# Performance work log

Hardware: AMD Instinct MI355X
Metric: run time of the kernel (lower is better)

## Reference

```python
import jax, jax.numpy as jnp
import numpy as np

B, F, D = 16384, 256, 128
H = [512, 256]
OUT = 8
VOCAB = 100000


def setup_inputs() -> dict:
    key = jax.random.key(0)
    ks = jax.random.split(key, 16)
    s = lambda k, *sh: jax.random.normal(k, sh, jnp.float32) * 0.05
    return dict(
        features=jax.random.normal(ks[0], (B, F), jnp.float32),
        ent_idx=jax.random.randint(ks[1], (B,), 0, VOCAB),
        target=jax.random.randint(ks[2], (B,), 0, OUT),
        Wf=s(ks[3], F, D), bf=jnp.zeros((D,), jnp.float32),
        Wu=s(ks[4], D, D), bu=jnp.zeros((D,), jnp.float32),
        w_cf=s(ks[5], D), w_fc=s(ks[6], D),
        w_ef=s(ks[7], D), w_fe=s(ks[8], D),
        b_c=jnp.zeros((1,), jnp.float32), b_e=jnp.zeros((1,), jnp.float32),
        head_tab=s(ks[9], VOCAB, D), ent_tab=s(ks[10], VOCAB, D),
        W0=s(ks[11], 2 * D, H[0]), b0=jnp.zeros((H[0],), jnp.float32),
        W1=s(ks[12], H[0], H[1]), b1=jnp.zeros((H[1],), jnp.float32),
        W2=s(ks[13], H[1], OUT), b2=jnp.zeros((OUT,), jnp.float32),
    )


def cross_compress(f, e, w_cf, w_fc, w_ef, w_fe, b_c, b_e):
    # torch code builds c = f (outer) e of shape (B,D,D) then matmuls a (D,1)
    # vector; algebraically (f e^T) w = f * (e . w), so we use the O(B*D) form.
    ew_cf = e @ w_cf  # (B,)
    fw_fc = f @ w_fc
    ew_ef = e @ w_ef
    fw_fe = f @ w_fe
    new_f = f * ew_cf[:, None] + e * fw_fc[:, None] + b_c
    new_e = f * ew_ef[:, None] + e * fw_fe[:, None] + b_e
    return new_f, new_e


def reference(features, ent_idx, target, Wf, bf, Wu, bu, w_cf, w_fc, w_ef,
              w_fe, b_c, b_e, head_tab, ent_tab, W0, b0, W1, b1, W2, b2):
    # 'rec' branch of CompanyOperationEvaluation.forward (eval mode, dropout=id)
    cf = jax.nn.relu(features @ Wf + bf)          # feature_layer
    e = ent_tab[ent_idx]                           # entity_embed lookup
    h = head_tab[ent_idx]                          # head_embed lookup (same ids)
    for _ in range(2):
        cf = jax.nn.relu(cf @ Wu + bu)             # user_low_mlp_layer
        h, e = cross_compress(h, e, w_cf, w_fc, w_ef, w_fe, b_c, b_e)
    high = jnp.concatenate([cf, e], axis=1)        # (B, 2D)
    x = jax.nn.relu(high @ W0 + b0)
    x = jax.nn.relu(x @ W1 + b1)
    x = jax.nn.relu(x @ W2 + b2)                   # pred_last_layer
    prob = jax.nn.softmax(x, axis=1)
    return (prob, target)
```

## Files before the change

### kernel.cpp

```cpp
#include <hip/hip_runtime.h>
#include <hip/hip_bf16.h>


typedef __bf16 bf16x8 __attribute__((ext_vector_type(8)));
typedef float floatx4 __attribute__((ext_vector_type(4)));

__device__ __forceinline__ unsigned short f2bf(float x) {
  unsigned int u = __builtin_bit_cast(unsigned int, x);
  u = (u + 0x7FFFu + ((u >> 16) & 1u)) >> 16;
  return (unsigned short)u;
}

__global__ __launch_bounds__(256) void prep_kernel(
    const int* __restrict__ ent_idx, const float* __restrict__ head_tab,
    const float* __restrict__ ent_tab,
    const float* __restrict__ w_cf, const float* __restrict__ w_fc,
    const float* __restrict__ w_ef, const float* __restrict__ w_fe,
    const float* __restrict__ b_c, const float* __restrict__ b_e,
    const float* __restrict__ Wf, const float* __restrict__ Wu,
    const float* __restrict__ W0, const float* __restrict__ W1,
    const float* __restrict__ W2,
    unsigned short* __restrict__ high,
    unsigned short* __restrict__ wfT, unsigned short* __restrict__ wuT,
    unsigned short* __restrict__ w0T, unsigned short* __restrict__ w1T,
    unsigned short* __restrict__ w2T) {
  __shared__ unsigned short tile[32][34];
  const int bid = blockIdx.x, tid = threadIdx.x;
  if (bid < 2048) {
    const int row = bid * 8 + (tid >> 5);
    const int c = (tid & 31) * 4;
    const int idx = ent_idx[row];
    float4 hv = *(const float4*)(head_tab + (size_t)idx * 128 + c);
    float4 ev = *(const float4*)(ent_tab + (size_t)idx * 128 + c);
    float h[4] = {hv.x, hv.y, hv.z, hv.w};
    float e[4] = {ev.x, ev.y, ev.z, ev.w};
    float wcf[4], wfc[4], wef[4], wfe[4];
#pragma unroll
    for (int j = 0; j < 4; ++j) {
      wcf[j] = w_cf[c + j]; wfc[j] = w_fc[c + j];
      wef[j] = w_ef[c + j]; wfe[j] = w_fe[c + j];
    }
    const float bc = b_c[0], be = b_e[0];
#pragma unroll
    for (int it = 0; it < 2; ++it) {
      float d0 = 0, d1 = 0, d2 = 0, d3 = 0;
#pragma unroll
      for (int j = 0; j < 4; ++j) {
        d0 += e[j] * wcf[j]; d1 += h[j] * wfc[j];
        d2 += e[j] * wef[j]; d3 += h[j] * wfe[j];
      }
#pragma unroll
      for (int s = 1; s < 32; s <<= 1) {
        d0 += __shfl_xor(d0, s); d1 += __shfl_xor(d1, s);
        d2 += __shfl_xor(d2, s); d3 += __shfl_xor(d3, s);
      }
      float nh[4], ne[4];
#pragma unroll
      for (int j = 0; j < 4; ++j) {
        nh[j] = h[j] * d0 + e[j] * d1 + bc;
        ne[j] = h[j] * d2 + e[j] * d3 + be;
      }
#pragma unroll
      for (int j = 0; j < 4; ++j) { h[j] = nh[j]; e[j] = ne[j]; }
    }
    uint2 v;
    v.x = (unsigned)f2bf(e[0]) | ((unsigned)f2bf(e[1]) << 16);
    v.y = (unsigned)f2bf(e[2]) | ((unsigned)f2bf(e[3]) << 16);
    *(uint2*)(high + (size_t)row * 256 + 128 + c) = v;
  } else if (bid < 2352) {
    int t = bid - 2048;
    const float* src; unsigned short* dst; int N, K, kt, nt;
    if (t < 32)       { src = Wf; dst = wfT; N = 128; K = 256; kt = t >> 2;       nt = t & 3; }
    else if (t < 48)  { t -= 32;  src = Wu; dst = wuT; N = 128; K = 128; kt = t >> 2; nt = t & 3; }
    else if (t < 176) { t -= 48;  src = W0; dst = w0T; N = 512; K = 256; kt = t >> 4; nt = t & 15; }
    else              { t -= 176; src = W1; dst = w1T; N = 256; K = 512; kt = t >> 3; nt = t & 7; }
    {
      int r = tid >> 3, cg = (tid & 7) * 4;
      float4 v = *(const float4*)(src + (size_t)(kt * 32 + r) * N + nt * 32 + cg);
      tile[r][cg + 0] = f2bf(v.x); tile[r][cg + 1] = f2bf(v.y);
      tile[r][cg + 2] = f2bf(v.z); tile[r][cg + 3] = f2bf(v.w);
    }
    __syncthreads();
    {
      int rp = tid >> 3, cg = (tid & 7) * 4;
      uint2 o;
      o.x = (unsigned)tile[cg + 0][rp] | ((unsigned)tile[cg + 1][rp] << 16);
      o.y = (unsigned)tile[cg + 2][rp] | ((unsigned)tile[cg + 3][rp] << 16);
      *(uint2*)(dst + (size_t)(nt * 32 + rp) * K + kt * 32 + cg) = o;
    }
  } else {
#pragma unroll
    for (int i = 0; i < 8; ++i) {
      int g = tid * 8 + i, k = g >> 3, n = g & 7;
      w2T[n * 256 + k] = f2bf(W2[g]);
    }
  }
}

template <int LDA>
__device__ __forceinline__ void layer32(const unsigned short* A_sh,
                                        const unsigned short* __restrict__ BT,
                                        int K, unsigned short* b_sh,
                                        floatx4 acc[2][2]) {
  const int tid = threadIdx.x, lane = tid & 63, wave = tid >> 6;
  const int m16 = lane & 15, quad = lane >> 4;
#pragma unroll
  for (int mi = 0; mi < 2; ++mi)
#pragma unroll
    for (int ni = 0; ni < 2; ++ni) acc[mi][ni] = (floatx4){0.f, 0.f, 0.f, 0.f};
  for (int k0 = 0; k0 < K; k0 += 64) {
    __syncthreads();
#pragma unroll
    for (int i = 0; i < 4; ++i) {
      int chunk = i * 256 + tid;
      int row = chunk >> 3, seg = chunk & 7;
      *(uint4*)&b_sh[row * 72 + seg * 8] =
          *(const uint4*)(BT + (size_t)row * K + k0 + seg * 8);
    }
    __syncthreads();
#pragma unroll
    for (int kk = 0; kk < 64; kk += 32) {
      bf16x8 a[2], b[2];
#pragma unroll
      for (int mi = 0; mi < 2; ++mi)
        a[mi] = *(const bf16x8*)&A_sh[(mi * 16 + m16) * LDA + k0 + kk + quad * 8];
#pragma unroll
      for (int ni = 0; ni < 2; ++ni)
        b[ni] = *(const bf16x8*)&b_sh[(wave * 32 + ni * 16 + m16) * 72 + kk + quad * 8];
#pragma unroll
      for (int mi = 0; mi < 2; ++mi)
#pragma unroll
        for (int ni = 0; ni < 2; ++ni)
          acc[mi][ni] = __builtin_amdgcn_mfma_f32_16x16x32_bf16(a[mi], b[ni], acc[mi][ni], 0, 0, 0);
    }
  }
  __syncthreads();
}

__global__ __launch_bounds__(256) void cf_chain_kernel(
    const float* __restrict__ features, const unsigned short* __restrict__ wfT,
    const unsigned short* __restrict__ wuT, const float* __restrict__ bf_,
    const float* __restrict__ bu, unsigned short* __restrict__ high) {
  __shared__ __align__(16) unsigned short feat_sh[32 * 264];
  __shared__ __align__(16) unsigned short buf0[32 * 136];
  __shared__ __align__(16) unsigned short buf1[32 * 136];
  __shared__ __align__(16) unsigned short b_sh[128 * 72];
  const int tid = threadIdx.x;
  const int r0 = blockIdx.x * 32;
#pragma unroll
  for (int i = 0; i < 8; ++i) {
    int idx4 = i * 256 + tid;
    int row = idx4 >> 6, c = (idx4 & 63) * 4;
    float4 v = *(const float4*)(features + (size_t)(r0 + row) * 256 + c);
    uint2 o;
    o.x = (unsigned)f2bf(v.x) | ((unsigned)f2bf(v.y) << 16);
    o.y = (unsigned)f2bf(v.z) | ((unsigned)f2bf(v.w) << 16);
    *(uint2*)&feat_sh[row * 264 + c] = o;
  }
  const int lane = tid & 63, wave = tid >> 6;
  const int m16 = lane & 15, quad = lane >> 4;
  floatx4 acc[2][2];

  layer32<264>(feat_sh, wfT, 256, b_sh, acc);
#pragma unroll
  for (int mi = 0; mi < 2; ++mi)
#pragma unroll
    for (int ni = 0; ni < 2; ++ni) {
      int col = wave * 32 + ni * 16 + m16;
      float bv = bf_[col];
#pragma unroll
      for (int r = 0; r < 4; ++r)
        buf0[(mi * 16 + quad * 4 + r) * 136 + col] =
            f2bf(fmaxf(acc[mi][ni][r] + bv, 0.f));
    }
  layer32<136>(buf0, wuT, 128, b_sh, acc);
#pragma unroll
  for (int mi = 0; mi < 2; ++mi)
#pragma unroll
    for (int ni = 0; ni < 2; ++ni) {
      int col = wave * 32 + ni * 16 + m16;
      float bv = bu[col];
#pragma unroll
      for (int r = 0; r < 4; ++r)
        buf1[(mi * 16 + quad * 4 + r) * 136 + col] =
            f2bf(fmaxf(acc[mi][ni][r] + bv, 0.f));
    }
  layer32<136>(buf1, wuT, 128, b_sh, acc);
#pragma unroll
  for (int mi = 0; mi < 2; ++mi)
#pragma unroll
    for (int ni = 0; ni < 2; ++ni) {
      int col = wave * 32 + ni * 16 + m16;
      float bv = bu[col];
#pragma unroll
      for (int r = 0; r < 4; ++r) {
        int row = r0 + mi * 16 + quad * 4 + r;
        high[(size_t)row * 256 + col] = f2bf(fmaxf(acc[mi][ni][r] + bv, 0.f));
      }
    }
}

__global__ __launch_bounds__(256) void gemm128_kernel(
    const unsigned short* __restrict__ A, const unsigned short* __restrict__ BT,
    const float* __restrict__ bias, unsigned short* __restrict__ C,
    int K, int ldc) {
  __shared__ __align__(16) unsigned short a_sh[128 * 72];
  __shared__ __align__(16) unsigned short b_sh[128 * 72];
  const int tid = threadIdx.x;
  const int bn = blockIdx.x, bm = blockIdx.y;
  const int lane = tid & 63;
  const int wave = tid >> 6;
  const int wm = wave & 1, wn = wave >> 1;
  const int m16 = lane & 15, quad = lane >> 4;

  floatx4 acc[4][4];
#pragma unroll
  for (int i = 0; i < 4; ++i)
#pragma unroll
    for (int j = 0; j < 4; ++j) acc[i][j] = (floatx4){0.f, 0.f, 0.f, 0.f};

  for (int k0 = 0; k0 < K; k0 += 64) {
    __syncthreads();
#pragma unroll
    for (int i = 0; i < 4; ++i) {
      int chunk = i * 256 + tid;
      int row = chunk >> 3, seg = chunk & 7;
      *(uint4*)&a_sh[row * 72 + seg * 8] =
          *(const uint4*)(A + (size_t)(bm * 128 + row) * K + k0 + seg * 8);
      *(uint4*)&b_sh[row * 72 + seg * 8] =
          *(const uint4*)(BT + (size_t)(bn * 128 + row) * K + k0 + seg * 8);
    }
    __syncthreads();
#pragma unroll
    for (int kk = 0; kk < 64; kk += 32) {
      bf16x8 af[4], bfr[4];
#pragma unroll
      for (int mi = 0; mi < 4; ++mi)
        af[mi] = *(const bf16x8*)&a_sh[(wm * 64 + mi * 16 + m16) * 72 + kk + quad * 8];
#pragma unroll
      for (int ni = 0; ni < 4; ++ni)
        bfr[ni] = *(const bf16x8*)&b_sh[(wn * 64 + ni * 16 + m16) * 72 + kk + quad * 8];
#pragma unroll
      for (int mi = 0; mi < 4; ++mi)
#pragma unroll
        for (int ni = 0; ni < 4; ++ni)
          acc[mi][ni] = __builtin_amdgcn_mfma_f32_16x16x32_bf16(
              af[mi], bfr[ni], acc[mi][ni], 0, 0, 0);
    }
  }
#pragma unroll
  for (int mi = 0; mi < 4; ++mi) {
#pragma unroll
    for (int ni = 0; ni < 4; ++ni) {
      int col = bn * 128 + wn * 64 + ni * 16 + m16;
      float bv = bias[col];
#pragma unroll
      for (int r = 0; r < 4; ++r) {
        int row = bm * 128 + wm * 64 + mi * 16 + quad * 4 + r;
        C[(size_t)row * ldc + col] = f2bf(fmaxf(acc[mi][ni][r] + bv, 0.f));
      }
    }
  }
}

__global__ __launch_bounds__(256) void gemm_w1_final_kernel(
    const unsigned short* __restrict__ x0, const unsigned short* __restrict__ w1T,
    const float* __restrict__ b1, const unsigned short* __restrict__ w2T,
    const float* __restrict__ b2, const int* __restrict__ target,
    float* __restrict__ out) {
  __shared__ __align__(16) unsigned short a_sh[32 * 72];
  __shared__ __align__(16) unsigned short b_sh[256 * 72];
  __shared__ __align__(16) unsigned short w2_sh[2048];
  unsigned short* x1_sh = b_sh;
  const int tid = threadIdx.x;
  const int r0 = blockIdx.x * 32;
  *(uint4*)&w2_sh[tid * 8] = *(const uint4*)(w2T + tid * 8);
  const int lane = tid & 63, wave = tid >> 6;
  const int m16 = lane & 15, quad = lane >> 4;
  floatx4 acc[2][4];
#pragma unroll
  for (int mi = 0; mi < 2; ++mi)
#pragma unroll
    for (int ni = 0; ni < 4; ++ni) acc[mi][ni] = (floatx4){0.f, 0.f, 0.f, 0.f};

  for (int k0 = 0; k0 < 512; k0 += 64) {
    __syncthreads();
    {
      int row = tid >> 3, seg = tid & 7;
      *(uint4*)&a_sh[row * 72 + seg * 8] =
          *(const uint4*)(x0 + (size_t)(r0 + row) * 512 + k0 + seg * 8);
    }
#pragma unroll
    for (int i = 0; i < 8; ++i) {
      int chunk = i * 256 + tid;
      int row = chunk >> 3, seg = chunk & 7;
      *(uint4*)&b_sh[row * 72 + seg * 8] =
          *(const uint4*)(w1T + (size_t)row * 512 + k0 + seg * 8);
    }
    __syncthreads();
#pragma unroll
    for (int kk = 0; kk < 64; kk += 32) {
      bf16x8 a[2], b[4];
#pragma unroll
      for (int mi = 0; mi < 2; ++mi)
        a[mi] = *(const bf16x8*)&a_sh[(mi * 16 + m16) * 72 + kk + quad * 8];
#pragma unroll
      for (int ni = 0; ni < 4; ++ni)
        b[ni] = *(const bf16x8*)&b_sh[(wave * 64 + ni * 16 + m16) * 72 + kk + quad * 8];
#pragma unroll
      for (int mi = 0; mi < 2; ++mi)
#pragma unroll
        for (int ni = 0; ni < 4; ++ni)
          acc[mi][ni] = __builtin_amdgcn_mfma_f32_16x16x32_bf16(a[mi], b[ni], acc[mi][ni], 0, 0, 0);
    }
  }
  __syncthreads();
#pragma unroll
  for (int mi = 0; mi < 2; ++mi)
#pragma unroll
    for (int ni = 0; ni < 4; ++ni) {
      int col = wave * 64 + ni * 16 + m16;
      float bv = b1[col];
#pragma unroll
      for (int r = 0; r < 4; ++r)
        x1_sh[(mi * 16 + quad * 4 + r) * 264 + col] = f2bf(fmaxf(acc[mi][ni][r] + bv, 0.f));
    }
  __syncthreads();
  {
    int row = tid >> 3, q = tid & 7;
    float p[8];
#pragma unroll
    for (int n = 0; n < 8; ++n) p[n] = 0.f;
#pragma unroll
    for (int jb = 0; jb < 4; ++jb) {
      bf16x8 xv = *(const bf16x8*)&x1_sh[row * 264 + q * 32 + jb * 8];
#pragma unroll
      for (int n = 0; n < 8; ++n) {
        bf16x8 wv = *(const bf16x8*)&w2_sh[n * 256 + q * 32 + jb * 8];
#pragma unroll
        for (int j = 0; j < 8; ++j) p[n] += (float)xv[j] * (float)wv[j];
      }
    }
#pragma unroll
    for (int s = 1; s < 8; s <<= 1)
#pragma unroll
      for (int n = 0; n < 8; ++n) p[n] += __shfl_xor(p[n], s);
    if (q == 0) {
      float mx = -1e30f;
#pragma unroll
      for (int n = 0; n < 8; ++n) {
        p[n] = fmaxf(p[n] + b2[n], 0.f);
        mx = fmaxf(mx, p[n]);
      }
      float sum = 0.f;
#pragma unroll
      for (int n = 0; n < 8; ++n) { p[n] = __expf(p[n] - mx); sum += p[n]; }
      const float inv = 1.f / sum;
      const int gr = r0 + row;
      float4 o0 = {p[0] * inv, p[1] * inv, p[2] * inv, p[3] * inv};
      float4 o1 = {p[4] * inv, p[5] * inv, p[6] * inv, p[7] * inv};
      *(float4*)(out + (size_t)gr * 8) = o0;
      *(float4*)(out + (size_t)gr * 8 + 4) = o1;
      out[16384 * 8 + gr] = (float)target[gr];
    }
  }
}

extern "C" void kernel_launch(void* const* d_in, const int* in_sizes, int n_in,
                              void* d_out, int out_size, void* d_ws, size_t ws_size,
                              hipStream_t stream) {
  const float* features = (const float*)d_in[0];
  const int* ent_idx    = (const int*)d_in[1];
  const int* target     = (const int*)d_in[2];
  const float* Wf  = (const float*)d_in[3];
  const float* bf_ = (const float*)d_in[4];
  const float* Wu  = (const float*)d_in[5];
  const float* bu  = (const float*)d_in[6];
  const float* w_cf = (const float*)d_in[7];
  const float* w_fc = (const float*)d_in[8];
  const float* w_ef = (const float*)d_in[9];
  const float* w_fe = (const float*)d_in[10];
  const float* b_c  = (const float*)d_in[11];
  const float* b_e  = (const float*)d_in[12];
  const float* head_tab = (const float*)d_in[13];
  const float* ent_tab  = (const float*)d_in[14];
  const float* W0 = (const float*)d_in[15];
  const float* b0 = (const float*)d_in[16];
  const float* W1 = (const float*)d_in[17];
  const float* b1 = (const float*)d_in[18];
  const float* W2 = (const float*)d_in[19];
  const float* b2 = (const float*)d_in[20];
  float* out = (float*)d_out;

  unsigned short* ws = (unsigned short*)d_ws;
  size_t off = 0;
  auto alloc = [&](size_t n) { unsigned short* p = ws + off; off += n; return p; };
  unsigned short* high = alloc(16384ull * 256);
  unsigned short* x0   = alloc(16384ull * 512);
  unsigned short* wfT  = alloc(32768);
  unsigned short* wuT  = alloc(16384);
  unsigned short* w0T  = alloc(131072);
  unsigned short* w1T  = alloc(131072);
  unsigned short* w2T  = alloc(2048);
  (void)ws_size; (void)in_sizes; (void)n_in; (void)out_size;

  prep_kernel<<<2353, 256, 0, stream>>>(ent_idx, head_tab, ent_tab,
      w_cf, w_fc, w_ef, w_fe, b_c, b_e, Wf, Wu, W0, W1, W2,
      high, wfT, wuT, w0T, w1T, w2T);
  cf_chain_kernel<<<512, 256, 0, stream>>>(features, wfT, wuT, bf_, bu, high);
  gemm128_kernel<<<dim3(4, 128), 256, 0, stream>>>(high, w0T, b0, x0, 256, 512);
  gemm_w1_final_kernel<<<512, 256, 0, stream>>>(x0, w1T, b1, w2T, b2, target, out);
}
```

Measured before the change: 191.0 us.

## Fuse cf chain, W0 GEMM and W1/final layers into one per-row-block kernel

Merges the cf_chain, W0 GEMM, and W1+softmax kernels into a single kernel working on 32-row blocks. The cf output and the x0 activations stay in shared memory instead of going through global memory, which removes the 16384x512 x0 round trip and two launches. The cost is that each block now reloads the full W0 and W1 weights from global/L2 with a small M tile (32 rows). Shared memory per block also grows, which may lower occupancy.

```diff
diff --git a/kernel.cpp b/kernel.cpp
--- a/kernel.cpp
+++ b/kernel.cpp
@@ -137,16 +137,28 @@
   __syncthreads();
 }
 
-__global__ __launch_bounds__(256) void cf_chain_kernel(
+__global__ __launch_bounds__(256) void fused_mlp_kernel(
     const float* __restrict__ features, const unsigned short* __restrict__ wfT,
     const unsigned short* __restrict__ wuT, const float* __restrict__ bf_,
-    const float* __restrict__ bu, unsigned short* __restrict__ high) {
-  __shared__ __align__(16) unsigned short feat_sh[32 * 264];
-  __shared__ __align__(16) unsigned short buf0[32 * 136];
-  __shared__ __align__(16) unsigned short buf1[32 * 136];
-  __shared__ __align__(16) unsigned short b_sh[128 * 72];
+    const float* __restrict__ bu, const unsigned short* __restrict__ high,
+    const unsigned short* __restrict__ w0T, const float* __restrict__ b0,
+    const unsigned short* __restrict__ w1T, const float* __restrict__ b1,
+    const unsigned short* __restrict__ w2T, const float* __restrict__ b2,
+    const int* __restrict__ target, float* __restrict__ out) {
+  __shared__ __align__(16) unsigned short regionA[17152];
+  __shared__ __align__(16) unsigned short b_sh[256 * 72];
+  __shared__ __align__(16) unsigned short w2_sh[2048];
+  unsigned short* feat_sh = regionA;
+  unsigned short* buf0 = regionA + 8448;
+  unsigned short* buf1 = regionA + 12800;
+  unsigned short* A_sh = regionA;
+  unsigned short* x0_sh = regionA;
+  unsigned short* x1_sh = b_sh;
+
   const int tid = threadIdx.x;
   const int r0 = blockIdx.x * 32;
+  *(uint4*)&w2_sh[tid * 8] = *(const uint4*)(w2T + tid * 8);
+
 #pragma unroll
   for (int i = 0; i < 8; ++i) {
     int idx4 = i * 256 + tid;
@@ -173,6 +185,13 @@
         buf0[(mi * 16 + quad * 4 + r) * 136 + col] =
             f2bf(fmaxf(acc[mi][ni][r] + bv, 0.f));
     }
+#pragma unroll
+  for (int i = 0; i < 2; ++i) {
+    int idx = i * 256 + tid;
+    int row = idx >> 4, seg = idx & 15;
+    *(uint4*)&A_sh[row * 264 + 128 + seg * 8] =
+        *(const uint4*)(high + (size_t)(r0 + row) * 256 + 128 + seg * 8);
+  }
   layer32<136>(buf0, wuT, 128, b_sh, acc);
 #pragma unroll
   for (int mi = 0; mi < 2; ++mi)
@@ -193,103 +212,68 @@
       int col = wave * 32 + ni * 16 + m16;
       float bv = bu[col];
 #pragma unroll
-      for (int r = 0; r < 4; ++r) {
-        int row = r0 + mi * 16 + quad * 4 + r;
-        high[(size_t)row * 256 + col] = f2bf(fmaxf(acc[mi][ni][r] + bv, 0.f));
-      }
-    }
-}
-
-__global__ __launch_bounds__(256) void gemm128_kernel(
-    const unsigned short* __restrict__ A, const unsigned short* __restrict__ BT,
-    const float* __restrict__ bias, unsigned short* __restrict__ C,
-    int K, int ldc) {
-  __shared__ __align__(16) unsigned short a_sh[128 * 72];
-  __shared__ __align__(16) unsigned short b_sh[128 * 72];
-  const int tid = threadIdx.x;
-  const int bn = blockIdx.x, bm = blockIdx.y;
-  const int lane = tid & 63;
-  const int wave = tid >> 6;
-  const int wm = wave & 1, wn = wave >> 1;
-  const int m16 = lane & 15, quad = lane >> 4;
-
-  floatx4 acc[4][4];
-#pragma unroll
-  for (int i = 0; i < 4; ++i)
-#pragma unroll
-    for (int j = 0; j < 4; ++j) acc[i][j] = (floatx4){0.f, 0.f, 0.f, 0.f};
-
-  for (int k0 = 0; k0 < K; k0 += 64) {
-    __syncthreads();
-#pragma unroll
-    for (int i = 0; i < 4; ++i) {
-      int chunk = i * 256 + tid;
-      int row = chunk >> 3, seg = chunk & 7;
-      *(uint4*)&a_sh[row * 72 + seg * 8] =
-          *(const uint4*)(A + (size_t)(bm * 128 + row) * K + k0 + seg * 8);
-      *(uint4*)&b_sh[row * 72 + seg * 8] =
-          *(const uint4*)(BT + (size_t)(bn * 128 + row) * K + k0 + seg * 8);
-    }
-    __syncthreads();
-#pragma unroll
-    for (int kk = 0; kk < 64; kk += 32) {
-      bf16x8 af[4], bfr[4];
-#pragma unroll
-      for (int mi = 0; mi < 4; ++mi)
-        af[mi] = *(const bf16x8*)&a_sh[(wm * 64 + mi * 16 + m16) * 72 + kk + quad * 8];
-#pragma unroll
-      for (int ni = 0; ni < 4; ++ni)
-        bfr[ni] = *(const bf16x8*)&b_sh[(wn * 64 + ni * 16 + m16) * 72 + kk + quad * 8];
-#pragma unroll
-      for (int mi = 0; mi < 4; ++mi)
+      for (int r = 0; r < 4; ++r)
+        A_sh[(mi * 16 + quad * 4 + r) * 264 + col] =
+            f2bf(fmaxf(acc[mi][ni][r] + bv, 0.f));
+    }
+
+  floatx4 acc8[2][8];
+#pragma unroll
+  for (int mi = 0; mi < 2; ++mi)
+#pragma unroll
+    for (int ni = 0; ni < 8; ++ni) acc8[mi][ni] = (floatx4){0.f, 0.f, 0.f, 0.f};
+  for (int k0 = 0; k0 < 256; k0 += 64) {
+#pragma unroll
+    for (int nh = 0; nh < 2; ++nh) {
+      __syncthreads();
+#pragma unroll
+      for (int i = 0; i < 8; ++i) {
+        int chunk = i * 256 + tid;
+        int row = chunk >> 3, seg = chunk & 7;
+        *(uint4*)&b_sh[row * 72 + seg * 8] =
+            *(const uint4*)(w0T + (size_t)(nh * 256 + row) * 256 + k0 + seg * 8);
+      }
+      __syncthreads();
+#pragma unroll
+      for (int kk = 0; kk < 64; kk += 32) {
+        bf16x8 a[2], b[4];
+#pragma unroll
+        for (int mi = 0; mi < 2; ++mi)
+          a[mi] = *(const bf16x8*)&A_sh[(mi * 16 + m16) * 264 + k0 + kk + quad * 8];
 #pragma unroll
         for (int ni = 0; ni < 4; ++ni)
-          acc[mi][ni] = __builtin_amdgcn_mfma_f32_16x16x32_bf16(
-              af[mi], bfr[ni], acc[mi][ni], 0, 0, 0);
-    }
-  }
-#pragma unroll
-  for (int mi = 0; mi < 4; ++mi) {
-#pragma unroll
-    for (int ni = 0; ni < 4; ++ni) {
-      int col = bn * 128 + wn * 64 + ni * 16 + m16;
-      float bv = bias[col];
-#pragma unroll
-      for (int r = 0; r < 4; ++r) {
-        int row = bm * 128 + wm * 64 + mi * 16 + quad * 4 + r;
-        C[(size_t)row * ldc + col] = f2bf(fmaxf(acc[mi][ni][r] + bv, 0.f));
-      }
-    }
-  }
-}
-
-__global__ __launch_bounds__(256) void gemm_w1_final_kernel(
-    const unsigned short* __restrict__ x0, const unsigned short* __restrict__ w1T,
-    const float* __restrict__ b1, const unsigned short* __restrict__ w2T,
-    const float* __restrict__ b2, const int* __restrict__ target,
-    float* __restrict__ out) {
-  __shared__ __align__(16) unsigned short a_sh[32 * 72];
-  __shared__ __align__(16) unsigned short b_sh[256 * 72];
-  __shared__ __align__(16) unsigned short w2_sh[2048];
-  unsigned short* x1_sh = b_sh;
-  const int tid = threadIdx.x;
-  const int r0 = blockIdx.x * 32;
-  *(uint4*)&w2_sh[tid * 8] = *(const uint4*)(w2T + tid * 8);
-  const int lane = tid & 63, wave = tid >> 6;
-  const int m16 = lane & 15, quad = lane >> 4;
-  floatx4 acc[2][4];
-#pragma unroll
-  for (int mi = 0; mi < 2; ++mi)
-#pragma unroll
-    for (int ni = 0; ni < 4; ++ni) acc[mi][ni] = (floatx4){0.f, 0.f, 0.f, 0.f};
-
+          b[ni] = *(const bf16x8*)&b_sh[(wave * 64 + ni * 16 + m16) * 72 + kk + quad * 8];
+#pragma unroll
+        for (int mi = 0; mi < 2; ++mi)
+#pragma unroll
+          for (int ni = 0; ni < 4; ++ni)
+            acc8[mi][nh * 4 + ni] = __builtin_amdgcn_mfma_f32_16x16x32_bf16(
+                a[mi], b[ni], acc8[mi][nh * 4 + ni], 0, 0, 0);
+      }
+    }
+  }
+  __syncthreads();
+#pragma unroll
+  for (int mi = 0; mi < 2; ++mi)
+#pragma unroll
+    for (int nh = 0; nh < 2; ++nh)
+#pragma unroll
+      for (int ni = 0; ni < 4; ++ni) {
+        int col = nh * 256 + wave * 64 + ni * 16 + m16;
+        float bv = b0[col];
+#pragma unroll
+        for (int r = 0; r < 4; ++r)
+          x0_sh[(mi * 16 + quad * 4 + r) * 520 + col] =
+              f2bf(fmaxf(acc8[mi][nh * 4 + ni][r] + bv, 0.f));
+      }
+
+  floatx4 acc4[2][4];
+#pragma unroll
+  for (int mi = 0; mi < 2; ++mi)
+#pragma unroll
+    for (int ni = 0; ni < 4; ++ni) acc4[mi][ni] = (floatx4){0.f, 0.f, 0.f, 0.f};
   for (int k0 = 0; k0 < 512; k0 += 64) {
     __syncthreads();
-    {
-      int row = tid >> 3, seg = tid & 7;
-      *(uint4*)&a_sh[row * 72 + seg * 8] =
-          *(const uint4*)(x0 + (size_t)(r0 + row) * 512 + k0 + seg * 8);
-    }
 #pragma unroll
     for (int i = 0; i < 8; ++i) {
       int chunk = i * 256 + tid;
@@ -303,7 +287,7 @@
       bf16x8 a[2], b[4];
 #pragma unroll
       for (int mi = 0; mi < 2; ++mi)
-        a[mi] = *(const bf16x8*)&a_sh[(mi * 16 + m16) * 72 + kk + quad * 8];
+        a[mi] = *(const bf16x8*)&x0_sh[(mi * 16 + m16) * 520 + k0 + kk + quad * 8];
 #pragma unroll
       for (int ni = 0; ni < 4; ++ni)
         b[ni] = *(const bf16x8*)&b_sh[(wave * 64 + ni * 16 + m16) * 72 + kk + quad * 8];
@@ -311,7 +295,7 @@
       for (int mi = 0; mi < 2; ++mi)
 #pragma unroll
         for (int ni = 0; ni < 4; ++ni)
-          acc[mi][ni] = __builtin_amdgcn_mfma_f32_16x16x32_bf16(a[mi], b[ni], acc[mi][ni], 0, 0, 0);
+          acc4[mi][ni] = __builtin_amdgcn_mfma_f32_16x16x32_bf16(a[mi], b[ni], acc4[mi][ni], 0, 0, 0);
     }
   }
   __syncthreads();
@@ -323,7 +307,7 @@
       float bv = b1[col];
 #pragma unroll
       for (int r = 0; r < 4; ++r)
-        x1_sh[(mi * 16 + quad * 4 + r) * 264 + col] = f2bf(fmaxf(acc[mi][ni][r] + bv, 0.f));
+        x1_sh[(mi * 16 + quad * 4 + r) * 264 + col] = f2bf(fmaxf(acc4[mi][ni][r] + bv, 0.f));
     }
   __syncthreads();
   {
@@ -396,7 +380,6 @@
   size_t off = 0;
   auto alloc = [&](size_t n) { unsigned short* p = ws + off; off += n; return p; };
   unsigned short* high = alloc(16384ull * 256);
-  unsigned short* x0   = alloc(16384ull * 512);
   unsigned short* wfT  = alloc(32768);
   unsigned short* wuT  = alloc(16384);
   unsigned short* w0T  = alloc(131072);
@@ -407,7 +390,6 @@
   prep_kernel<<<2353, 256, 0, stream>>>(ent_idx, head_tab, ent_tab,
       w_cf, w_fc, w_ef, w_fe, b_c, b_e, Wf, Wu, W0, W1, W2,
       high, wfT, wuT, w0T, w1T, w2T);
-  cf_chain_kernel<<<512, 256, 0, stream>>>(features, wfT, wuT, bf_, bu, high);
-  gemm128_kernel<<<dim3(4, 128), 256, 0, stream>>>(high, w0T, b0, x0, 256, 512);
-  gemm_w1_final_kernel<<<512, 256, 0, stream>>>(x0, w1T, b1, w2T, b2, target, out);
-}
+  fused_mlp_kernel<<<512, 256, 0, stream>>>(features, wfT, wuT, bf_, bu,
+      high, w0T, b0, w1T, b1, w2T, b2, target, out);
+}
```

New measurement: 202.6 us. 1.06x slower.
